# Optimization experiments

Measured on AMD Instinct MI355X. Metric: run time of the kernel, lower is better.

## Reference

```python
import jax, jax.numpy as jnp
import numpy as np

N_NODES = 100_000
N_EDGES = 3_200_000  # avg in-degree 32
N_CLASSES = 16
TEMP = 0.5


def setup_inputs() -> dict:
    key = jax.random.key(0)
    k1, k2, k3 = jax.random.split(key, 3)
    src = jax.random.randint(k1, (N_EDGES,), 0, N_NODES, dtype=jnp.int32)
    # guarantee every node has at least one incoming edge so scatter-mean
    # and the sharpening normalization are well-defined
    dst = jnp.concatenate([
        jnp.arange(N_NODES, dtype=jnp.int32),
        jax.random.randint(k2, (N_EDGES - N_NODES,), 0, N_NODES, dtype=jnp.int32),
    ])
    edge_index = jnp.stack([src, dst], axis=0)  # [2, E]
    # positive predictions (log is taken downstream)
    aug_pred = jax.random.uniform(k3, (N_NODES, N_CLASSES), jnp.float32, 1e-3, 1.0)
    return {"edge_index": edge_index, "aug_pred": aug_pred}


def reference(edge_index, aug_pred):
    src = edge_index[0]  # message source nodes
    dst = edge_index[1]  # aggregation targets
    E = edge_index.shape[1]

    # scatter-mean aggregation: avg_pred[i] = mean_{e: dst[e]=i} aug_pred[src[e]]
    msg = aug_pred[src]                                   # [E, C]
    sums = jax.ops.segment_sum(msg, dst, num_segments=N_NODES)
    cnt = jax.ops.segment_sum(jnp.ones((E,), aug_pred.dtype), dst,
                              num_segments=N_NODES)
    avg_pred = sums / jnp.maximum(cnt, 1.0)[:, None]      # [N, C]

    # temperature sharpening + normalize
    p = avg_pred ** (1.0 / TEMP)
    sharp_avg_pred = p / jnp.sum(p, axis=1, keepdims=True)

    # edge-indexed gathers; dst side is detached in the original
    s = (avg_pred + 1e-10)[src]                            # [E, C]
    d = jax.lax.stop_gradient(sharp_avg_pred + 1e-10)[dst]  # [E, C]

    cr_loss = (d * jnp.log(d) - d * jnp.log(s)).sum(axis=1)  # [E]
    return cr_loss.mean()
```

## Files before the change

kernel.cpp:

```cpp
#include <hip/hip_runtime.h>

#define NCLS 16
#define NB 391
#define BSH 8
#define TILE 4096
#define BTHR 512
#define KPT 8
#define PREB 512
#define BMAX 9216
#define ACAP 9

static __device__ __forceinline__ float bflo(unsigned u) {
  return __uint_as_float(u << 16);
}
static __device__ __forceinline__ float bfhi(unsigned u) {
  return __uint_as_float(u & 0xFFFF0000u);
}
static __device__ __forceinline__ unsigned f2bf1(float f) {
  unsigned u = __float_as_uint(f);
  return (u + 0x7FFF + ((u >> 16) & 1)) >> 16;
}
static __device__ __forceinline__ unsigned packbf(float a, float b) {
  return f2bf1(a) | (f2bf1(b) << 16);
}

__global__ void pre_kernel(const int* __restrict__ dstv, int* __restrict__ bcnt, int E,
                           const float2* __restrict__ aug, unsigned* __restrict__ augh, int n2) {
  __shared__ int lh[NB];
  if (blockIdx.x < PREB) {
    for (int t = threadIdx.x; t < NB; t += 256) lh[t] = 0;
    __syncthreads();
    int stride = PREB * 256;
    for (int i = blockIdx.x * 256 + threadIdx.x; i < E; i += stride)
      atomicAdd(&lh[dstv[i] >> BSH], 1);
    __syncthreads();
    for (int t = threadIdx.x; t < NB; t += 256) {
      int v = lh[t];
      if (v) atomicAdd(&bcnt[t], v);
    }
  } else {
    int i = (blockIdx.x - PREB) * 256 + threadIdx.x;
    if (i < n2) {
      float2 v = aug[i];
      augh[i] = packbf(v.x, v.y);
    }
  }
}

__global__ void bscan_kernel(const int* __restrict__ bcnt, int* __restrict__ bbase,
                             int* __restrict__ gcur) {
  __shared__ int tmp[512];
  int t = threadIdx.x;
  int x = (t < NB) ? bcnt[t] : 0;
  tmp[t] = x;
  __syncthreads();
  for (int o = 1; o < 512; o <<= 1) {
    int v = (t >= o) ? tmp[t - o] : 0;
    __syncthreads();
    tmp[t] += v;
    __syncthreads();
  }
  if (t < NB) { int e = tmp[t] - x; bbase[t] = e; gcur[t] = e; }
  if (t == NB - 1) bbase[NB] = tmp[t];
}

__global__ void __launch_bounds__(BTHR) bin_kernel(const int* __restrict__ srcv,
                                                   const int* __restrict__ dstv,
                                                   int* __restrict__ gcur,
                                                   int* __restrict__ packed, int E) {
  __shared__ int hist[NB];
  __shared__ int off[NB];
  __shared__ int delta[NB];
  __shared__ int part[16];
  __shared__ int2 stag[TILE];
  int tid = threadIdx.x;
  int base = blockIdx.x * TILE;
  int cnt = min(TILE, E - base);
  for (int t = tid; t < NB; t += BTHR) hist[t] = 0;
  __syncthreads();
  int myw[KPT];
  int myp[KPT];
#pragma unroll
  for (int k = 0; k < KPT; k++) {
    int idx = tid + k * BTHR;
    myw[k] = -1;
    myp[k] = 0;
    if (idx < cnt) {
      int s = srcv[base + idx], d = dstv[base + idx];
      int b = d >> BSH;
      int r = atomicAdd(&hist[b], 1);
      myw[k] = s | ((d & 255) << 17);
      myp[k] = (b << 12) | r;
    }
  }
  __syncthreads();
  if (tid < 16) {
    int s = 0;
    int lo = tid * 25, hiX = min(NB, lo + 25);
    for (int j = lo; j < hiX; j++) { int v = hist[j]; off[j] = s; s += v; }
    part[tid] = s;
  }
  __syncthreads();
  if (tid == 0) {
    int run = 0;
    for (int j = 0; j < 16; j++) { int v = part[j]; part[j] = run; run += v; }
  }
  __syncthreads();
  for (int t = tid; t < NB; t += BTHR) off[t] += part[t / 25];
  __syncthreads();
  for (int t = tid; t < NB; t += BTHR) {
    int c = hist[t];
    int gb = c ? atomicAdd(&gcur[t], c) : 0;
    delta[t] = gb - off[t];
  }
  __syncthreads();
#pragma unroll
  for (int k = 0; k < KPT; k++) {
    if (myw[k] >= 0) {
      int b = myp[k] >> 12, r = myp[k] & 4095;
      int p = off[b] + r;
      int2 w;
      w.x = myw[k];
      w.y = p + delta[b];
      stag[p] = w;
    }
  }
  __syncthreads();
  for (int i = tid; i < cnt; i += BTHR) {
    int2 w = stag[i];
    packed[w.y] = w.x;
  }
}

__global__ void __launch_bounds__(1024) agg_kernel(const int* __restrict__ bbase,
                                                   const int* __restrict__ packed,
                                                   const unsigned* __restrict__ augh,
                                                   unsigned* __restrict__ logs,
                                                   float* __restrict__ dvec,
                                                   double* __restrict__ acc, int N) {
  __shared__ int ssrc[BMAX];
  __shared__ int hist[256];
  __shared__ int off[256];
  __shared__ float red[16];
  int tid = threadIdx.x;
  int b = blockIdx.x;
  int rbeg = bbase[b], rend = bbase[b + 1];
  if (tid < 256) hist[tid] = 0;
  __syncthreads();
  int myw[ACAP];
  int myr[ACAP];
#pragma unroll
  for (int k = 0; k < ACAP; k++) {
    int i = rbeg + tid + k * 1024;
    int w = (i < rend) ? packed[i] : -1;
    myw[k] = w;
    myr[k] = (w >= 0) ? atomicAdd(&hist[w >> 17], 1) : 0;
  }
  __syncthreads();
  if (tid < 64) {
    int h0 = hist[4 * tid], h1 = hist[4 * tid + 1];
    int h2 = hist[4 * tid + 2], h3 = hist[4 * tid + 3];
    int tot = h0 + h1 + h2 + h3;
    int inc = tot;
#pragma unroll
    for (int o = 1; o < 64; o <<= 1) {
      int u = __shfl_up(inc, o, 64);
      if (tid >= o) inc += u;
    }
    int exc = inc - tot;
    off[4 * tid] = exc;
    off[4 * tid + 1] = exc + h0;
    off[4 * tid + 2] = exc + h0 + h1;
    off[4 * tid + 3] = exc + h0 + h1 + h2;
  }
  __syncthreads();
#pragma unroll
  for (int k = 0; k < ACAP; k++) {
    int w = myw[k];
    if (w >= 0) ssrc[off[w >> 17] + myr[k]] = w & 0x1FFFF;
  }
  __syncthreads();
  int node = tid >> 2, lane = tid & 3;
  int boff = off[node];
  int deg = hist[node];
  double s0 = 0., s1 = 0., s2 = 0., s3 = 0.;
  int wsh = lane << 1;
  int e = 0;
  for (; e + 8 <= deg; e += 8) {
    int q0 = ssrc[boff + e],     q1 = ssrc[boff + e + 1];
    int q2 = ssrc[boff + e + 2], q3 = ssrc[boff + e + 3];
    int q4 = ssrc[boff + e + 4], q5 = ssrc[boff + e + 5];
    int q6 = ssrc[boff + e + 6], q7 = ssrc[boff + e + 7];
    uint2 g0 = *reinterpret_cast<const uint2*>(augh + ((size_t)q0 << 3) + wsh);
    uint2 g1 = *reinterpret_cast<const uint2*>(augh + ((size_t)q1 << 3) + wsh);
    uint2 g2 = *reinterpret_cast<const uint2*>(augh + ((size_t)q2 << 3) + wsh);
    uint2 g3 = *reinterpret_cast<const uint2*>(augh + ((size_t)q3 << 3) + wsh);
    uint2 g4 = *reinterpret_cast<const uint2*>(augh + ((size_t)q4 << 3) + wsh);
    uint2 g5 = *reinterpret_cast<const uint2*>(augh + ((size_t)q5 << 3) + wsh);
    uint2 g6 = *reinterpret_cast<const uint2*>(augh + ((size_t)q6 << 3) + wsh);
    uint2 g7 = *reinterpret_cast<const uint2*>(augh + ((size_t)q7 << 3) + wsh);
    s0 += (double)bflo(g0.x) + (double)bflo(g1.x) + (double)bflo(g2.x) + (double)bflo(g3.x) +
          (double)bflo(g4.x) + (double)bflo(g5.x) + (double)bflo(g6.x) + (double)bflo(g7.x);
    s1 += (double)bfhi(g0.x) + (double)bfhi(g1.x) + (double)bfhi(g2.x) + (double)bfhi(g3.x) +
          (double)bfhi(g4.x) + (double)bfhi(g5.x) + (double)bfhi(g6.x) + (double)bfhi(g7.x);
    s2 += (double)bflo(g0.y) + (double)bflo(g1.y) + (double)bflo(g2.y) + (double)bflo(g3.y) +
          (double)bflo(g4.y) + (double)bflo(g5.y) + (double)bflo(g6.y) + (double)bflo(g7.y);
    s3 += (double)bfhi(g0.y) + (double)bfhi(g1.y) + (double)bfhi(g2.y) + (double)bfhi(g3.y) +
          (double)bfhi(g4.y) + (double)bfhi(g5.y) + (double)bfhi(g6.y) + (double)bfhi(g7.y);
  }
  for (; e < deg; e++) {
    int q0 = ssrc[boff + e];
    uint2 g0 = *reinterpret_cast<const uint2*>(augh + ((size_t)q0 << 3) + wsh);
    s0 += (double)bflo(g0.x); s1 += (double)bfhi(g0.x);
    s2 += (double)bflo(g0.y); s3 += (double)bfhi(g0.y);
  }
  double dinv = 1.0 / (double)(deg > 0 ? deg : 1);
  float a0 = (float)(s0 * dinv), a1 = (float)(s1 * dinv);
  float a2 = (float)(s2 * dinv), a3 = (float)(s3 * dinv);
  float p2 = a0 * a0 + a1 * a1 + a2 * a2 + a3 * a3;
  p2 += __shfl_xor(p2, 1, 64);
  p2 += __shfl_xor(p2, 2, 64);
  float ip = 1.0f / p2;
  float d0 = a0 * a0 * ip + 1e-10f, d1 = a1 * a1 * ip + 1e-10f;
  float d2 = a2 * a2 * ip + 1e-10f, d3 = a3 * a3 * ip + 1e-10f;
  float h = d0 * __logf(d0) + d1 * __logf(d1) + d2 * __logf(d2) + d3 * __logf(d3);
  h += __shfl_xor(h, 1, 64);
  h += __shfl_xor(h, 2, 64);
  int g = (b << BSH) + node;
  float contrib = 0.f;
  if (g < N) {
    uint2 lw;
    lw.x = packbf(__logf(a0 + 1e-10f), __logf(a1 + 1e-10f));
    lw.y = packbf(__logf(a2 + 1e-10f), __logf(a3 + 1e-10f));
    *reinterpret_cast<uint2*>(logs + ((size_t)g << 3) + wsh) = lw;
    float4 dd;
    dd.x = d0; dd.y = d1; dd.z = d2; dd.w = d3;
    *reinterpret_cast<float4*>(dvec + ((size_t)g << 4) + (lane << 2)) = dd;
    if (lane == 0) contrib = (float)deg * h;
  }
#pragma unroll
  for (int o = 32; o >= 1; o >>= 1) contrib += __shfl_xor(contrib, o, 64);
  if ((tid & 63) == 0) red[tid >> 6] = contrib;
  __syncthreads();
  if (tid == 0) {
    float s = 0.f;
#pragma unroll
    for (int wv = 0; wv < 16; wv++) s += red[wv];
    atomicAdd(acc, (double)s);
  }
}

#define ASTR 17
__global__ void __launch_bounds__(1024) loss_kernel(const int* __restrict__ bbase,
                                                    const int* __restrict__ packed,
                                                    const unsigned* __restrict__ logs,
                                                    const float* __restrict__ dvec,
                                                    double* __restrict__ acc,
                                                    int* __restrict__ done,
                                                    float* __restrict__ out,
                                                    int N, int E) {
  __shared__ float sdv[256 * ASTR];
  __shared__ double red[16];
  int tid = threadIdx.x;
  int b = blockIdx.x;
  int rbeg = bbase[b], rend = bbase[b + 1];
  int nb0 = b << BSH;
  {
    const float4* gsrc = reinterpret_cast<const float4*>(dvec + ((size_t)nb0 << 4));
    int nvalid = min(256, N - nb0);
    int nf4 = nvalid * 4;
    for (int i = tid; i < nf4; i += 1024) {
      float4 v = gsrc[i];
      float* r = sdv + (i >> 2) * ASTR + ((i & 3) << 2);
      r[0] = v.x; r[1] = v.y; r[2] = v.z; r[3] = v.w;
    }
  }
  __syncthreads();
  double dot = 0.0;
  int i = rbeg + tid;
  for (; i + 1024 < rend; i += 2048) {
    int wa = packed[i];
    int wb = packed[i + 1024];
    int sa = wa & 0x1FFFF, la = wa >> 17;
    int sb = wb & 0x1FFFF, lb = wb >> 17;
    const uint4* ga = reinterpret_cast<const uint4*>(logs + ((size_t)sa << 3));
    const uint4* gb = reinterpret_cast<const uint4*>(logs + ((size_t)sb << 3));
    uint4 a0 = ga[0], a1 = ga[1];
    uint4 b0 = gb[0], b1 = gb[1];
    const float* ra = sdv + la * ASTR;
    const float* rb = sdv + lb * ASTR;
    float ea = ra[0] * bflo(a0.x) + ra[1] * bfhi(a0.x) +
               ra[2] * bflo(a0.y) + ra[3] * bfhi(a0.y) +
               ra[4] * bflo(a0.z) + ra[5] * bfhi(a0.z) +
               ra[6] * bflo(a0.w) + ra[7] * bfhi(a0.w) +
               ra[8] * bflo(a1.x) + ra[9] * bfhi(a1.x) +
               ra[10] * bflo(a1.y) + ra[11] * bfhi(a1.y) +
               ra[12] * bflo(a1.z) + ra[13] * bfhi(a1.z) +
               ra[14] * bflo(a1.w) + ra[15] * bfhi(a1.w);
    float eb = rb[0] * bflo(b0.x) + rb[1] * bfhi(b0.x) +
               rb[2] * bflo(b0.y) + rb[3] * bfhi(b0.y) +
               rb[4] * bflo(b0.z) + rb[5] * bfhi(b0.z) +
               rb[6] * bflo(b0.w) + rb[7] * bfhi(b0.w) +
               rb[8] * bflo(b1.x) + rb[9] * bfhi(b1.x) +
               rb[10] * bflo(b1.y) + rb[11] * bfhi(b1.y) +
               rb[12] * bflo(b1.z) + rb[13] * bfhi(b1.z) +
               rb[14] * bflo(b1.w) + rb[15] * bfhi(b1.w);
    dot += (double)ea + (double)eb;
  }
  if (i < rend) {
    int wa = packed[i];
    int sa = wa & 0x1FFFF, la = wa >> 17;
    const uint4* ga = reinterpret_cast<const uint4*>(logs + ((size_t)sa << 3));
    uint4 a0 = ga[0], a1 = ga[1];
    const float* ra = sdv + la * ASTR;
    float ea = ra[0] * bflo(a0.x) + ra[1] * bfhi(a0.x) +
               ra[2] * bflo(a0.y) + ra[3] * bfhi(a0.y) +
               ra[4] * bflo(a0.z) + ra[5] * bfhi(a0.z) +
               ra[6] * bflo(a0.w) + ra[7] * bfhi(a0.w) +
               ra[8] * bflo(a1.x) + ra[9] * bfhi(a1.x) +
               ra[10] * bflo(a1.y) + ra[11] * bfhi(a1.y) +
               ra[12] * bflo(a1.z) + ra[13] * bfhi(a1.z) +
               ra[14] * bflo(a1.w) + ra[15] * bfhi(a1.w);
    dot += (double)ea;
  }
#pragma unroll
  for (int o = 32; o >= 1; o >>= 1) dot += __shfl_xor(dot, o, 64);
  if ((tid & 63) == 0) red[tid >> 6] = dot;
  __syncthreads();
  if (tid == 0) {
    double s = 0.0;
#pragma unroll
    for (int wv = 0; wv < 16; wv++) s += red[wv];
    atomicAdd(acc, -s);
    __threadfence();
    int t = atomicAdd(done, 1);
    if (t == (int)gridDim.x - 1) {
      double v = atomicAdd(acc, 0.0);
      out[0] = (float)(v / (double)E);
    }
  }
}

extern "C" void kernel_launch(void* const* d_in, const int* in_sizes, int n_in,
                              void* d_out, int out_size, void* d_ws, size_t ws_size,
                              hipStream_t stream) {
  const int* edge_index = (const int*)d_in[0];
  const float* aug_pred = (const float*)d_in[1];
  const int E = in_sizes[0] / 2;
  const int N = in_sizes[1] / NCLS;

  const int* srcv = edge_index;
  const int* dstv = edge_index + E;

  char* p = (char*)d_ws;
  auto alloc = [&](size_t bytes) {
    char* r = p;
    p += (bytes + 255) & ~(size_t)255;
    return r;
  };
  double* acc = (double*)alloc(8);
  int* bcnt = (int*)alloc(NB * 4);
  int* done = (int*)alloc(4);
  int* bbase = (int*)alloc((NB + 1) * 4);
  int* gcur = (int*)alloc(NB * 4);
  int* packed = (int*)alloc((size_t)E * 4);
  unsigned* augh = (unsigned*)alloc((size_t)N * NCLS * 2);
  unsigned* logs = (unsigned*)alloc((size_t)N * NCLS * 2);
  float* dvec = (float*)alloc((size_t)N * NCLS * 4);

  size_t zero_bytes = (size_t)((char*)bbase - (char*)d_ws);
  hipMemsetAsync(d_ws, 0, zero_bytes, stream);

  int n2 = N * NCLS / 2;
  int cvtb = (n2 + 255) / 256;
  pre_kernel<<<PREB + cvtb, 256, 0, stream>>>(dstv, bcnt, E, (const float2*)aug_pred, augh, n2);
  bscan_kernel<<<1, 512, 0, stream>>>(bcnt, bbase, gcur);
  int tiles = (E + TILE - 1) / TILE;
  bin_kernel<<<tiles, BTHR, 0, stream>>>(srcv, dstv, gcur, packed, E);
  agg_kernel<<<NB, 1024, 0, stream>>>(bbase, packed, augh, logs, dvec, acc, N);
  loss_kernel<<<NB, 1024, 0, stream>>>(bbase, packed, logs, dvec, acc, done,
                                       (float*)d_out, N, E);
}
```

Baseline: 175.4 us.

## Replace bin count and scan pre-pass with fixed-capacity per-bin buckets

Removes the pre-pass histogram kernel and the single-block scan kernel. Each destination bin now gets a fixed slot of CAP entries in the packed buffer, and the per-bin atomic cursor (gcur) doubles as the bin count read by the aggregation and loss kernels. The bf16 conversion of predictions is folded into the binning kernel. This saves a full read of the dst array and two kernel launches, but it assumes no bin exceeds CAP edges and pads the packed buffer.

```diff
diff --git a/kernel.cpp b/kernel.cpp
--- a/kernel.cpp
+++ b/kernel.cpp
@@ -6,9 +6,8 @@
 #define TILE 4096
 #define BTHR 512
 #define KPT 8
-#define PREB 512
-#define BMAX 9216
-#define ACAP 9
+#define CAP 10240
+#define ACAP 10
 
 static __device__ __forceinline__ float bflo(unsigned u) {
   return __uint_as_float(u << 16);
@@ -24,56 +23,23 @@
   return f2bf1(a) | (f2bf1(b) << 16);
 }
 
-__global__ void pre_kernel(const int* __restrict__ dstv, int* __restrict__ bcnt, int E,
-                           const float2* __restrict__ aug, unsigned* __restrict__ augh, int n2) {
-  __shared__ int lh[NB];
-  if (blockIdx.x < PREB) {
-    for (int t = threadIdx.x; t < NB; t += 256) lh[t] = 0;
-    __syncthreads();
-    int stride = PREB * 256;
-    for (int i = blockIdx.x * 256 + threadIdx.x; i < E; i += stride)
-      atomicAdd(&lh[dstv[i] >> BSH], 1);
-    __syncthreads();
-    for (int t = threadIdx.x; t < NB; t += 256) {
-      int v = lh[t];
-      if (v) atomicAdd(&bcnt[t], v);
-    }
-  } else {
-    int i = (blockIdx.x - PREB) * 256 + threadIdx.x;
-    if (i < n2) {
-      float2 v = aug[i];
-      augh[i] = packbf(v.x, v.y);
-    }
-  }
-}
-
-__global__ void bscan_kernel(const int* __restrict__ bcnt, int* __restrict__ bbase,
-                             int* __restrict__ gcur) {
-  __shared__ int tmp[512];
-  int t = threadIdx.x;
-  int x = (t < NB) ? bcnt[t] : 0;
-  tmp[t] = x;
-  __syncthreads();
-  for (int o = 1; o < 512; o <<= 1) {
-    int v = (t >= o) ? tmp[t - o] : 0;
-    __syncthreads();
-    tmp[t] += v;
-    __syncthreads();
-  }
-  if (t < NB) { int e = tmp[t] - x; bbase[t] = e; gcur[t] = e; }
-  if (t == NB - 1) bbase[NB] = tmp[t];
-}
-
 __global__ void __launch_bounds__(BTHR) bin_kernel(const int* __restrict__ srcv,
                                                    const int* __restrict__ dstv,
+                                                   const float2* __restrict__ aug,
+                                                   unsigned* __restrict__ augh,
                                                    int* __restrict__ gcur,
-                                                   int* __restrict__ packed, int E) {
+                                                   int* __restrict__ packed,
+                                                   int E, int n2) {
   __shared__ int hist[NB];
   __shared__ int off[NB];
   __shared__ int delta[NB];
   __shared__ int part[16];
   __shared__ int2 stag[TILE];
   int tid = threadIdx.x;
+  for (int i = blockIdx.x * BTHR + tid; i < n2; i += gridDim.x * BTHR) {
+    float2 v = aug[i];
+    augh[i] = packbf(v.x, v.y);
+  }
   int base = blockIdx.x * TILE;
   int cnt = min(TILE, E - base);
   for (int t = tid; t < NB; t += BTHR) hist[t] = 0;
@@ -111,7 +77,7 @@
   for (int t = tid; t < NB; t += BTHR) {
     int c = hist[t];
     int gb = c ? atomicAdd(&gcur[t], c) : 0;
-    delta[t] = gb - off[t];
+    delta[t] = t * CAP + gb - off[t];
   }
   __syncthreads();
 #pragma unroll
@@ -132,27 +98,28 @@
   }
 }
 
-__global__ void __launch_bounds__(1024) agg_kernel(const int* __restrict__ bbase,
+__global__ void __launch_bounds__(1024) agg_kernel(const int* __restrict__ gcur,
                                                    const int* __restrict__ packed,
                                                    const unsigned* __restrict__ augh,
                                                    unsigned* __restrict__ logs,
                                                    float* __restrict__ dvec,
                                                    double* __restrict__ acc, int N) {
-  __shared__ int ssrc[BMAX];
+  __shared__ int ssrc[CAP];
   __shared__ int hist[256];
   __shared__ int off[256];
   __shared__ float red[16];
   int tid = threadIdx.x;
   int b = blockIdx.x;
-  int rbeg = bbase[b], rend = bbase[b + 1];
+  int rbeg = b * CAP;
+  int cnt = gcur[b];
   if (tid < 256) hist[tid] = 0;
   __syncthreads();
   int myw[ACAP];
   int myr[ACAP];
 #pragma unroll
   for (int k = 0; k < ACAP; k++) {
-    int i = rbeg + tid + k * 1024;
-    int w = (i < rend) ? packed[i] : -1;
+    int i = tid + k * 1024;
+    int w = (i < cnt) ? packed[rbeg + i] : -1;
     myw[k] = w;
     myr[k] = (w >= 0) ? atomicAdd(&hist[w >> 17], 1) : 0;
   }
@@ -251,7 +218,7 @@
 }
 
 #define ASTR 17
-__global__ void __launch_bounds__(1024) loss_kernel(const int* __restrict__ bbase,
+__global__ void __launch_bounds__(1024) loss_kernel(const int* __restrict__ gcur,
                                                     const int* __restrict__ packed,
                                                     const unsigned* __restrict__ logs,
                                                     const float* __restrict__ dvec,
@@ -263,7 +230,9 @@
   __shared__ double red[16];
   int tid = threadIdx.x;
   int b = blockIdx.x;
-  int rbeg = bbase[b], rend = bbase[b + 1];
+  int rbeg = b * CAP;
+  int cnt = gcur[b];
+  int rend = rbeg + cnt;
   int nb0 = b << BSH;
   {
     const float4* gsrc = reinterpret_cast<const float4*>(dvec + ((size_t)nb0 << 4));
@@ -359,25 +328,21 @@
     return r;
   };
   double* acc = (double*)alloc(8);
-  int* bcnt = (int*)alloc(NB * 4);
   int* done = (int*)alloc(4);
-  int* bbase = (int*)alloc((NB + 1) * 4);
   int* gcur = (int*)alloc(NB * 4);
-  int* packed = (int*)alloc((size_t)E * 4);
+  int* packed = (int*)alloc((size_t)NB * CAP * 4);
   unsigned* augh = (unsigned*)alloc((size_t)N * NCLS * 2);
   unsigned* logs = (unsigned*)alloc((size_t)N * NCLS * 2);
   float* dvec = (float*)alloc((size_t)N * NCLS * 4);
 
-  size_t zero_bytes = (size_t)((char*)bbase - (char*)d_ws);
+  size_t zero_bytes = (size_t)((char*)packed - (char*)d_ws);
   hipMemsetAsync(d_ws, 0, zero_bytes, stream);
 
   int n2 = N * NCLS / 2;
-  int cvtb = (n2 + 255) / 256;
-  pre_kernel<<<PREB + cvtb, 256, 0, stream>>>(dstv, bcnt, E, (const float2*)aug_pred, augh, n2);
-  bscan_kernel<<<1, 512, 0, stream>>>(bcnt, bbase, gcur);
   int tiles = (E + TILE - 1) / TILE;
-  bin_kernel<<<tiles, BTHR, 0, stream>>>(srcv, dstv, gcur, packed, E);
-  agg_kernel<<<NB, 1024, 0, stream>>>(bbase, packed, augh, logs, dvec, acc, N);
-  loss_kernel<<<NB, 1024, 0, stream>>>(bbase, packed, logs, dvec, acc, done,
+  bin_kernel<<<tiles, BTHR, 0, stream>>>(srcv, dstv, (const float2*)aug_pred,
+                                         augh, gcur, packed, E, n2);
+  agg_kernel<<<NB, 1024, 0, stream>>>(gcur, packed, augh, logs, dvec, acc, N);
+  loss_kernel<<<NB, 1024, 0, stream>>>(gcur, packed, logs, dvec, acc, done,
                                        (float*)d_out, N, E);
 }
```

Result: faster. 156.6 us (-10.7%).
